# Kernel optimization log

Hardware: AMD Instinct MI355X
Metric: run time of the kernel (lower is better)

Reference implementation:

```python
import jax, jax.numpy as jnp
import numpy as np

HID, H, QR, KVR, DN, DR, DV = 2048, 20, 768, 512, 192, 64, 256
HEAD_DIM = DN + DR  # 256
EPS = 1e-5
THETA = 1000000.0
SCALE = 1.0 / np.sqrt(HEAD_DIM)


def rmsnorm(x, w):
    rms = jnp.sqrt(jnp.mean(x * x, axis=-1, keepdims=True) + EPS)
    return x / rms * w


def rope_apply(x, positions):
    # x: [B,S,H,DR], positions: [B,S] int
    inv_freq = 1.0 / (THETA ** (jnp.arange(0, DR, 2, dtype=jnp.float32) / DR))  # [DR/2]
    freqs = positions.astype(jnp.float32)[..., None] * inv_freq  # [B,S,DR/2]
    cos = jnp.cos(freqs)[:, :, None, :]  # [B,S,1,DR/2]
    sin = jnp.sin(freqs)[:, :, None, :]
    x1, x2 = x[..., ::2], x[..., 1::2]
    return jnp.concatenate([x1 * cos - x2 * sin, x1 * sin + x2 * cos], axis=-1)


def setup_inputs() -> dict:
    key = jax.random.key(0)
    ks = jax.random.split(key, 7)
    B, S = 1, 2048
    return {
        "x": jax.random.normal(ks[0], (B, S, HID), dtype=jnp.float32),
        "positions": jnp.tile(jnp.arange(S, dtype=jnp.int32)[None, :], (B, 1)),
        "q_a_w": jax.random.normal(ks[1], (QR, HID), dtype=jnp.float32) * 0.02,
        "q_b_w": jax.random.normal(ks[2], (H * HEAD_DIM, QR), dtype=jnp.float32) * 0.02,
        "kv_a_w": jax.random.normal(ks[3], (KVR + DR, HID), dtype=jnp.float32) * 0.02,
        "kv_b_w": jax.random.normal(ks[4], (H * (DN + DV), KVR), dtype=jnp.float32) * 0.02,
        "o_w": jax.random.normal(ks[5], (HID, H * DV), dtype=jnp.float32) * 0.02,
        "q_a_ln_w": jnp.ones((QR,), dtype=jnp.float32),
        "kv_a_ln_w": jnp.ones((KVR,), dtype=jnp.float32),
    }


def reference(x, positions, q_a_w, q_b_w, kv_a_w, kv_b_w, o_w, q_a_ln_w, kv_a_ln_w):
    B, S, _ = x.shape
    # Q: LoRA down -> RMSNorm -> up
    q = rmsnorm(x @ q_a_w.T, q_a_ln_w) @ q_b_w.T  # [B,S,H*HEAD_DIM]
    q = q.reshape(B, S, H, HEAD_DIM)
    # KV: compressed projection, split lora / rope-pe parts
    kv_c = x @ kv_a_w.T  # [B,S,KVR+DR]
    kv_lora, k_rope_pe = kv_c[..., :KVR], kv_c[..., KVR:]
    kv_exp = rmsnorm(kv_lora, kv_a_ln_w) @ kv_b_w.T  # [B,S,H*(DN+DV)]
    kv_exp = kv_exp.reshape(B, S, H, DN + DV)
    k_nope, v = kv_exp[..., :DN], kv_exp[..., DN:]
    k_rope = jnp.broadcast_to(k_rope_pe[:, :, None, :], (B, S, H, DR))
    q_nope, q_rope = q[..., :DN], q[..., DN:]
    q_rope = rope_apply(q_rope, positions)
    k_rope = rope_apply(k_rope, positions)
    qf = jnp.concatenate([q_nope, q_rope], axis=-1)  # [B,S,H,HEAD_DIM]
    kf = jnp.concatenate([k_nope, k_rope], axis=-1)
    # attention: manual matmul-softmax-matmul
    attn = jnp.einsum("bqhd,bkhd->bhqk", qf, kf) * SCALE
    attn = jax.nn.softmax(attn, axis=-1)
    out = jnp.einsum("bhqk,bkhd->bqhd", attn, v).reshape(B, S, H * DV)
    return out @ o_w.T
```

## Files before the change

### kernel.cpp

```cpp
#include <hip/hip_runtime.h>
#include <hip/hip_bf16.h>

#define HID 2048
#define NH 20
#define QR 768
#define KVR 512
#define DN 192
#define DR 64
#define DV 256
#define HD 256
#define S_LEN 2048
#define HKV 448
#define KV_N (NH * HKV)
#define Q_N (NH * HD)
#define O_N (NH * DV)
#define KVA_N (KVR + DR)
#define KVAP 640
#define QKVA (QR + KVAP)

typedef short bf16x8 __attribute__((ext_vector_type(8)));
typedef short bf16x4 __attribute__((ext_vector_type(4)));
typedef float f32x4 __attribute__((ext_vector_type(4)));

__device__ inline short f2bs(float f) {
  __hip_bfloat16 h = __float2bfloat16(f);
  return *reinterpret_cast<short*>(&h);
}
__device__ inline float bs2f(short s) {
  __hip_bfloat16 h = *reinterpret_cast<__hip_bfloat16*>(&s);
  return __bfloat162float(h);
}

__device__ inline void gload16(const void* g, void* l) {
  __builtin_amdgcn_global_load_lds((const __attribute__((address_space(1))) void*)g,
                                   (__attribute__((address_space(3))) void*)l, 16, 0, 0);
}

#define WAIT_VM0() asm volatile("s_waitcnt vmcnt(0)" ::: "memory")

__global__ void f2b_kernel(const float* __restrict__ in, short* __restrict__ out, size_t n8) {
  size_t i = (size_t)blockIdx.x * blockDim.x + threadIdx.x;
  size_t stride = (size_t)gridDim.x * blockDim.x;
  for (; i < n8; i += stride) {
    f32x4 a = *(const f32x4*)(in + i * 8);
    f32x4 b = *(const f32x4*)(in + i * 8 + 4);
    bf16x8 r;
    r[0] = f2bs(a[0]); r[1] = f2bs(a[1]); r[2] = f2bs(a[2]); r[3] = f2bs(a[3]);
    r[4] = f2bs(b[0]); r[5] = f2bs(b[1]); r[6] = f2bs(b[2]); r[7] = f2bs(b[3]);
    *(bf16x8*)(out + i * 8) = r;
  }
}

template <int OUT_BF16>
__global__ __launch_bounds__(256) void gemm128(const short* __restrict__ A,
                                               const short* __restrict__ B,
                                               void* __restrict__ Cp,
                                               int M, int N, int K) {
  __shared__ alignas(16) short As[128 * 64];
  __shared__ alignas(16) short Bs[128 * 64];
  int tid = threadIdx.x;
  int w = tid >> 6, l = tid & 63;
  int lr = l & 15, lg = l >> 4;
  int wr = w >> 1, wc = w & 1;
  int row0 = blockIdx.y * 128, col0 = blockIdx.x * 128;
  f32x4 acc[4][4] = {};
  for (int k0 = 0; k0 < K; k0 += 64) {
    if (k0) __syncthreads();
#pragma unroll
    for (int p = 0; p < 4; ++p) {
      int c = p * 256 + tid;
      int row = c >> 3;
      int sb = ((c & 7) * 16) ^ ((row & 7) << 4);
      gload16((const char*)A + ((size_t)(row0 + row) * K + k0) * 2 + sb, (char*)As + c * 16);
      gload16((const char*)B + ((size_t)(col0 + row) * K + k0) * 2 + sb, (char*)Bs + c * 16);
    }
    __syncthreads();
    bf16x8 af[4][2], bf[4][2];
#pragma unroll
    for (int m = 0; m < 4; ++m)
#pragma unroll
      for (int kk = 0; kk < 2; ++kk) {
        int ra = wr * 64 + m * 16 + lr;
        int rb = wc * 64 + m * 16 + lr;
        int cb = kk * 64 + lg * 16;
        af[m][kk] = *(const bf16x8*)((const char*)As + ra * 128 + (cb ^ ((ra & 7) << 4)));
        bf[m][kk] = *(const bf16x8*)((const char*)Bs + rb * 128 + (cb ^ ((rb & 7) << 4)));
      }
#pragma unroll
    for (int m = 0; m < 4; ++m)
#pragma unroll
      for (int n = 0; n < 4; ++n) {
        acc[m][n] = __builtin_amdgcn_mfma_f32_16x16x32_bf16(af[m][0], bf[n][0], acc[m][n], 0, 0, 0);
        acc[m][n] = __builtin_amdgcn_mfma_f32_16x16x32_bf16(af[m][1], bf[n][1], acc[m][n], 0, 0, 0);
      }
  }
#pragma unroll
  for (int m = 0; m < 4; ++m)
#pragma unroll
    for (int n = 0; n < 4; ++n)
#pragma unroll
      for (int r = 0; r < 4; ++r) {
        int row = row0 + wr * 64 + m * 16 + lg * 4 + r;
        int col = col0 + wc * 64 + n * 16 + lr;
        if (OUT_BF16)
          ((short*)Cp)[(size_t)row * N + col] = f2bs(acc[m][n][r]);
        else
          ((float*)Cp)[(size_t)row * N + col] = acc[m][n][r];
      }
}

__global__ __launch_bounds__(256) void gemm64(const short* __restrict__ A,
                                              const short* __restrict__ B,
                                              float* __restrict__ C,
                                              int M, int N, int K) {
  __shared__ alignas(16) short As[64 * 64];
  __shared__ alignas(16) short Bs[128 * 64];
  int tid = threadIdx.x;
  int w = tid >> 6, l = tid & 63;
  int lr = l & 15, lg = l >> 4;
  int wr = w >> 1, wc = w & 1;
  int row0 = blockIdx.y * 64, col0 = blockIdx.x * 128;
  f32x4 acc[2][4] = {};
  for (int k0 = 0; k0 < K; k0 += 64) {
    if (k0) __syncthreads();
#pragma unroll
    for (int p = 0; p < 2; ++p) {
      int c = p * 256 + tid;
      int row = c >> 3;
      int sb = ((c & 7) * 16) ^ ((row & 7) << 4);
      gload16((const char*)A + ((size_t)(row0 + row) * K + k0) * 2 + sb, (char*)As + c * 16);
    }
#pragma unroll
    for (int p = 0; p < 4; ++p) {
      int c = p * 256 + tid;
      int row = c >> 3;
      int sb = ((c & 7) * 16) ^ ((row & 7) << 4);
      gload16((const char*)B + ((size_t)(col0 + row) * K + k0) * 2 + sb, (char*)Bs + c * 16);
    }
    __syncthreads();
    bf16x8 af[2][2], bf[4][2];
#pragma unroll
    for (int m = 0; m < 2; ++m)
#pragma unroll
      for (int kk = 0; kk < 2; ++kk) {
        int ra = wr * 32 + m * 16 + lr;
        int cb = kk * 64 + lg * 16;
        af[m][kk] = *(const bf16x8*)((const char*)As + ra * 128 + (cb ^ ((ra & 7) << 4)));
      }
#pragma unroll
    for (int n = 0; n < 4; ++n)
#pragma unroll
      for (int kk = 0; kk < 2; ++kk) {
        int rb = wc * 64 + n * 16 + lr;
        int cb = kk * 64 + lg * 16;
        bf[n][kk] = *(const bf16x8*)((const char*)Bs + rb * 128 + (cb ^ ((rb & 7) << 4)));
      }
#pragma unroll
    for (int m = 0; m < 2; ++m)
#pragma unroll
      for (int n = 0; n < 4; ++n) {
        acc[m][n] = __builtin_amdgcn_mfma_f32_16x16x32_bf16(af[m][0], bf[n][0], acc[m][n], 0, 0, 0);
        acc[m][n] = __builtin_amdgcn_mfma_f32_16x16x32_bf16(af[m][1], bf[n][1], acc[m][n], 0, 0, 0);
      }
  }
#pragma unroll
  for (int m = 0; m < 2; ++m)
#pragma unroll
    for (int n = 0; n < 4; ++n)
#pragma unroll
      for (int r = 0; r < 4; ++r) {
        int row = row0 + wr * 32 + m * 16 + lg * 4 + r;
        int col = col0 + wc * 64 + n * 16 + lr;
        C[(size_t)row * N + col] = acc[m][n][r];
      }
}

__global__ __launch_bounds__(256) void rmsnorm_kernel(const float* __restrict__ in,
                                                      const float* __restrict__ w,
                                                      short* __restrict__ out,
                                                      int N, int in_stride, int out_stride) {
  int row = blockIdx.x;
  const float* x = in + (size_t)row * in_stride;
  float ss = 0.f;
  for (int i = threadIdx.x * 4; i < N; i += 1024) {
    f32x4 v = *(const f32x4*)(x + i);
    ss += v[0] * v[0] + v[1] * v[1] + v[2] * v[2] + v[3] * v[3];
  }
#pragma unroll
  for (int off = 32; off >= 1; off >>= 1) ss += __shfl_down(ss, off);
  __shared__ float red[4];
  if ((threadIdx.x & 63) == 0) red[threadIdx.x >> 6] = ss;
  __syncthreads();
  float tot = red[0] + red[1] + red[2] + red[3];
  float sc = rsqrtf(tot / (float)N + 1e-5f);
  short* o = out + (size_t)row * out_stride;
  for (int i = threadIdx.x * 4; i < N; i += 1024) {
    f32x4 v = *(const f32x4*)(x + i);
    f32x4 g = *(const f32x4*)(w + i);
    bf16x4 r;
    r[0] = f2bs(v[0] * sc * g[0]); r[1] = f2bs(v[1] * sc * g[1]);
    r[2] = f2bs(v[2] * sc * g[2]); r[3] = f2bs(v[3] * sc * g[3]);
    *(bf16x4*)(o + i) = r;
  }
}

__global__ void rope_table_kernel(const int* __restrict__ pos, float* __restrict__ ct,
                                  float* __restrict__ st) {
  int s = blockIdx.x * blockDim.x + threadIdx.x;
  if (s >= S_LEN) return;
  double p = (double)pos[s];
  for (int d = 0; d < 32; ++d) {
    double invf = exp(-((double)(2 * d) / 64.0) * log(1.0e6));
    double a = p * invf;
    ct[s * 32 + d] = (float)cos(a);
    st[s * 32 + d] = (float)sin(a);
  }
}

__global__ void rope_q_kernel(short* __restrict__ q, const float* __restrict__ ct,
                              const float* __restrict__ st) {
  int idx = blockIdx.x * blockDim.x + threadIdx.x;
  if (idx >= S_LEN * NH) return;
  int s = idx / NH, h = idx % NH;
  short* p = q + (size_t)s * Q_N + h * HD + DN;
  bf16x8 v[8];
#pragma unroll
  for (int j = 0; j < 8; ++j) v[j] = *(const bf16x8*)(p + j * 8);
  float x[64];
#pragma unroll
  for (int j = 0; j < 8; ++j)
#pragma unroll
    for (int k = 0; k < 8; ++k) x[j * 8 + k] = bs2f(v[j][k]);
  const float* c = ct + s * 32;
  const float* sn = st + s * 32;
  bf16x8 o[8];
#pragma unroll
  for (int d = 0; d < 32; ++d) {
    float cd = c[d], sd = sn[d];
    float x1 = x[2 * d], x2 = x[2 * d + 1];
    o[d >> 3][d & 7] = f2bs(x1 * cd - x2 * sd);
    o[4 + (d >> 3)][d & 7] = f2bs(x1 * sd + x2 * cd);
  }
#pragma unroll
  for (int j = 0; j < 8; ++j) *(bf16x8*)(p + j * 8) = o[j];
}

__global__ void rope_k_kernel(const float* __restrict__ base, const float* __restrict__ ct,
                              const float* __restrict__ st, short* __restrict__ kr) {
  int s = blockIdx.x * blockDim.x + threadIdx.x;
  if (s >= S_LEN) return;
  const float* xp = base + (size_t)s * QKVA;
  float x[64];
#pragma unroll
  for (int j = 0; j < 16; ++j) {
    f32x4 v = *(const f32x4*)(xp + j * 4);
    x[j * 4] = v[0]; x[j * 4 + 1] = v[1]; x[j * 4 + 2] = v[2]; x[j * 4 + 3] = v[3];
  }
  const float* c = ct + s * 32;
  const float* sn = st + s * 32;
  bf16x8 o[8];
#pragma unroll
  for (int d = 0; d < 32; ++d) {
    float cd = c[d], sd = sn[d];
    float x1 = x[2 * d], x2 = x[2 * d + 1];
    o[d >> 3][d & 7] = f2bs(x1 * cd - x2 * sd);
    o[4 + (d >> 3)][d & 7] = f2bs(x1 * sd + x2 * cd);
  }
  short* kp = kr + s * 64;
#pragma unroll
  for (int j = 0; j < 8; ++j) *(bf16x8*)(kp + j * 8) = o[j];
}

__global__ void kc_build(const short* __restrict__ kvx, const short* __restrict__ kr,
                         short* __restrict__ kc) {
  int idx = blockIdx.x * 256 + threadIdx.x;
  int h = idx >> 16;
  int r = idx & 65535;
  int s = r >> 5, c = r & 31;
  const short* src = (c < 24) ? kvx + (size_t)s * KV_N + h * HKV + c * 8
                              : kr + (size_t)s * 64 + (c - 24) * 8;
  *(bf16x8*)(kc + ((size_t)h * S_LEN + s) * HD + c * 8) = *(const bf16x8*)src;
}

__global__ __launch_bounds__(256) void vtrans(const short* __restrict__ kvx,
                                              short* __restrict__ vtg) {
  __shared__ short tile[64][65];
  int s0 = blockIdx.x * 64, d0 = blockIdx.y * 64, h = blockIdx.z;
  int tid = threadIdx.x;
#pragma unroll
  for (int p = 0; p < 2; ++p) {
    int s = p * 32 + (tid >> 3), dc = (tid & 7) * 8;
    bf16x8 v = *(const bf16x8*)(kvx + (size_t)(s0 + s) * KV_N + h * HKV + DN + d0 + dc);
#pragma unroll
    for (int j = 0; j < 8; ++j) tile[s][dc + j] = v[j];
  }
  __syncthreads();
#pragma unroll
  for (int p = 0; p < 2; ++p) {
    int d = p * 32 + (tid >> 3), sc = (tid & 7) * 8;
    bf16x4 a, b;
#pragma unroll
    for (int j = 0; j < 4; ++j) a[j] = tile[sc + j][d];
#pragma unroll
    for (int j = 0; j < 4; ++j) b[j] = tile[sc + 4 + j][d];
    int q1 = sc & 31, q2 = q1 + 4;
    int p1 = (q1 < 16) ? (q1 >> 2) * 8 : ((q1 - 16) >> 2) * 8 + 4;
    int p2 = (q2 < 16) ? (q2 >> 2) * 8 : ((q2 - 16) >> 2) * 8 + 4;
    int s = ((d & 15) >> 1) & 3;
    p1 = ((((p1 >> 3) ^ s)) << 3) | (p1 & 7);
    p2 = ((((p2 >> 3) ^ s)) << 3) | (p2 & 7);
    size_t rowbase = ((size_t)h * DV + d0 + d) * S_LEN + s0 + (sc & ~31);
    *(bf16x4*)(vtg + rowbase + p1) = a;
    *(bf16x4*)(vtg + rowbase + p2) = b;
  }
}

__global__ __launch_bounds__(256, 2) void attn10(const short* __restrict__ q,
                                                 const short* __restrict__ kc,
                                                 const short* __restrict__ vtg,
                                                 short* __restrict__ out) {
  __shared__ alignas(16) short ks[2][32 * 256];
  __shared__ alignas(16) short vt[2][256 * 32];
  int bid = blockIdx.x;
  int swz = (bid & 7) * 40 + (bid >> 3);
  int h = swz >> 4, qblk = swz & 15;
  int tid = threadIdx.x;
  int w = tid >> 6, l = tid & 63;
  int lr = l & 15, lg = l >> 4;

  const char* kch = (const char*)(kc + (size_t)h * S_LEN * HD);
  const short* vth = vtg + (size_t)h * DV * S_LEN;

  int qrowA = qblk * 128 + w * 32 + lr;
  const short* qbA = q + (size_t)qrowA * Q_N + h * HD;
  const short* qbB = qbA + (size_t)16 * Q_N;
  bf16x8 qfA[8], qfB[8];
#pragma unroll
  for (int kk = 0; kk < 8; ++kk) {
    bf16x8 va = *(const bf16x8*)(qbA + kk * 32 + lg * 8);
    bf16x8 vb = *(const bf16x8*)(qbB + kk * 32 + lg * 8);
#pragma unroll
    for (int j = 0; j < 8; ++j) {
      va[j] = f2bs(bs2f(va[j]) * 0.0625f);
      vb[j] = f2bs(bs2f(vb[j]) * 0.0625f);
    }
    qfA[kk] = va;
    qfB[kk] = vb;
  }

  f32x4 accA[16] = {}, accB[16] = {};
  float mA = -3e38f, mB = -3e38f;
  float lsA = 0.f, lsB = 0.f;

  auto stage_k = [&](int buf, int key0) {
#pragma unroll
    for (int p = 0; p < 4; ++p) {
      int c = p * 256 + tid;
      int row = c >> 5;
      int sb = ((c & 31) * 16) ^ ((row & 7) << 4);
      gload16(kch + (size_t)(key0 + row) * 512 + sb, (char*)ks[buf] + c * 16);
    }
  };
  auto stage_v = [&](int buf, int key0) {
#pragma unroll
    for (int p = 0; p < 4; ++p) {
      int c = p * 256 + tid;
      int d = c >> 2, slot = c & 3;
      gload16(vth + (size_t)d * S_LEN + key0 + slot * 8, (char*)vt[buf] + c * 16);
    }
  };

  stage_k(0, 0);
  stage_v(0, 0);
  WAIT_VM0();
  __builtin_amdgcn_s_barrier();

  int sxor = (lr >> 1) & 3;

  for (int kb = 0; kb < S_LEN / 32; ++kb) {
    int cur = kb & 1;
    int key0 = kb * 32;
    if (kb + 1 < S_LEN / 32) {
      stage_k(cur ^ 1, key0 + 32);
      stage_v(cur ^ 1, key0 + 32);
    }

    f32x4 s0A = {}, s1A = {}, s0B = {}, s1B = {};
    __builtin_amdgcn_s_setprio(1);
#pragma unroll
    for (int kk = 0; kk < 8; ++kk) {
      int cb = kk * 64 + lg * 16;
      int sw = (lr & 7) << 4;
      bf16x8 k0 = *(const bf16x8*)((const char*)ks[cur] + lr * 512 + (cb ^ sw));
      bf16x8 k1 = *(const bf16x8*)((const char*)ks[cur] + (16 + lr) * 512 + (cb ^ sw));
      s0A = __builtin_amdgcn_mfma_f32_16x16x32_bf16(k0, qfA[kk], s0A, 0, 0, 0);
      s1A = __builtin_amdgcn_mfma_f32_16x16x32_bf16(k1, qfA[kk], s1A, 0, 0, 0);
      s0B = __builtin_amdgcn_mfma_f32_16x16x32_bf16(k0, qfB[kk], s0B, 0, 0, 0);
      s1B = __builtin_amdgcn_mfma_f32_16x16x32_bf16(k1, qfB[kk], s1B, 0, 0, 0);
    }
    __builtin_amdgcn_s_setprio(0);

    bf16x8 paA, paB;
    {
      float mx = fmaxf(fmaxf(fmaxf(s0A[0], s0A[1]), fmaxf(s0A[2], s0A[3])),
                       fmaxf(fmaxf(s1A[0], s1A[1]), fmaxf(s1A[2], s1A[3])));
      mx = fmaxf(mx, __shfl_xor(mx, 16));
      mx = fmaxf(mx, __shfl_xor(mx, 32));
      bool grow = mx > mA + 8.f;
      if (__any((int)grow)) {
        float mn = fmaxf(mA, mx);
        float co = __expf(mA - mn);
        mA = mn;
        lsA *= co;
        float c0 = __shfl(co, (l & 48) | (lg * 4 + 0));
        float c1 = __shfl(co, (l & 48) | (lg * 4 + 1));
        float c2 = __shfl(co, (l & 48) | (lg * 4 + 2));
        float c3 = __shfl(co, (l & 48) | (lg * 4 + 3));
#pragma unroll
        for (int t = 0; t < 16; ++t) {
          accA[t][0] *= c0; accA[t][1] *= c1; accA[t][2] *= c2; accA[t][3] *= c3;
        }
      }
      float e0 = __expf(s0A[0] - mA), e1 = __expf(s0A[1] - mA);
      float e2 = __expf(s0A[2] - mA), e3 = __expf(s0A[3] - mA);
      float e4 = __expf(s1A[0] - mA), e5 = __expf(s1A[1] - mA);
      float e6 = __expf(s1A[2] - mA), e7 = __expf(s1A[3] - mA);
      float ts = ((e0 + e1) + (e2 + e3)) + ((e4 + e5) + (e6 + e7));
      ts += __shfl_xor(ts, 16);
      ts += __shfl_xor(ts, 32);
      lsA += ts;
      paA[0] = f2bs(e0); paA[1] = f2bs(e1); paA[2] = f2bs(e2); paA[3] = f2bs(e3);
      paA[4] = f2bs(e4); paA[5] = f2bs(e5); paA[6] = f2bs(e6); paA[7] = f2bs(e7);
    }
    {
      float mx = fmaxf(fmaxf(fmaxf(s0B[0], s0B[1]), fmaxf(s0B[2], s0B[3])),
                       fmaxf(fmaxf(s1B[0], s1B[1]), fmaxf(s1B[2], s1B[3])));
      mx = fmaxf(mx, __shfl_xor(mx, 16));
      mx = fmaxf(mx, __shfl_xor(mx, 32));
      bool grow = mx > mB + 8.f;
      if (__any((int)grow)) {
        float mn = fmaxf(mB, mx);
        float co = __expf(mB - mn);
        mB = mn;
        lsB *= co;
        float c0 = __shfl(co, (l & 48) | (lg * 4 + 0));
        float c1 = __shfl(co, (l & 48) | (lg * 4 + 1));
        float c2 = __shfl(co, (l & 48) | (lg * 4 + 2));
        float c3 = __shfl(co, (l & 48) | (lg * 4 + 3));
#pragma unroll
        for (int t = 0; t < 16; ++t) {
          accB[t][0] *= c0; accB[t][1] *= c1; accB[t][2] *= c2; accB[t][3] *= c3;
        }
      }
      float e0 = __expf(s0B[0] - mB), e1 = __expf(s0B[1] - mB);
      float e2 = __expf(s0B[2] - mB), e3 = __expf(s0B[3] - mB);
      float e4 = __expf(s1B[0] - mB), e5 = __expf(s1B[1] - mB);
      float e6 = __expf(s1B[2] - mB), e7 = __expf(s1B[3] - mB);
      float ts = ((e0 + e1) + (e2 + e3)) + ((e4 + e5) + (e6 + e7));
      ts += __shfl_xor(ts, 16);
      ts += __shfl_xor(ts, 32);
      lsB += ts;
      paB[0] = f2bs(e0); paB[1] = f2bs(e1); paB[2] = f2bs(e2); paB[3] = f2bs(e3);
      paB[4] = f2bs(e4); paB[5] = f2bs(e5); paB[6] = f2bs(e6); paB[7] = f2bs(e7);
    }

    __builtin_amdgcn_s_setprio(1);
#pragma unroll
    for (int t = 0; t < 16; ++t) {
      int d = t * 16 + lr;
      bf16x8 vf = *(const bf16x8*)((const char*)vt[cur] + d * 64 + ((lg ^ sxor) << 4));
      accA[t] = __builtin_amdgcn_mfma_f32_16x16x32_bf16(paA, vf, accA[t], 0, 0, 0);
      accB[t] = __builtin_amdgcn_mfma_f32_16x16x32_bf16(paB, vf, accB[t], 0, 0, 0);
    }
    __builtin_amdgcn_s_setprio(0);

    WAIT_VM0();
    __builtin_amdgcn_s_barrier();
  }

  {
    float inv = 1.f / lsA;
    float i0 = __shfl(inv, (l & 48) | (lg * 4 + 0));
    float i1 = __shfl(inv, (l & 48) | (lg * 4 + 1));
    float i2 = __shfl(inv, (l & 48) | (lg * 4 + 2));
    float i3 = __shfl(inv, (l & 48) | (lg * 4 + 3));
#pragma unroll
    for (int t = 0; t < 16; ++t) {
      int row = qblk * 128 + w * 32 + lg * 4;
      int col = h * DV + t * 16 + lr;
      out[(size_t)(row + 0) * O_N + col] = f2bs(accA[t][0] * i0);
      out[(size_t)(row + 1) * O_N + col] = f2bs(accA[t][1] * i1);
      out[(size_t)(row + 2) * O_N + col] = f2bs(accA[t][2] * i2);
      out[(size_t)(row + 3) * O_N + col] = f2bs(accA[t][3] * i3);
    }
  }
  {
    float inv = 1.f / lsB;
    float i0 = __shfl(inv, (l & 48) | (lg * 4 + 0));
    float i1 = __shfl(inv, (l & 48) | (lg * 4 + 1));
    float i2 = __shfl(inv, (l & 48) | (lg * 4 + 2));
    float i3 = __shfl(inv, (l & 48) | (lg * 4 + 3));
#pragma unroll
    for (int t = 0; t < 16; ++t) {
      int row = qblk * 128 + w * 32 + 16 + lg * 4;
      int col = h * DV + t * 16 + lr;
      out[(size_t)(row + 0) * O_N + col] = f2bs(accB[t][0] * i0);
      out[(size_t)(row + 1) * O_N + col] = f2bs(accB[t][1] * i1);
      out[(size_t)(row + 2) * O_N + col] = f2bs(accB[t][2] * i2);
      out[(size_t)(row + 3) * O_N + col] = f2bs(accB[t][3] * i3);
    }
  }
}

extern "C" void kernel_launch(void* const* d_in, const int* in_sizes, int n_in,
                              void* d_out, int out_size, void* d_ws, size_t ws_size,
                              hipStream_t stream) {
  const float* x       = (const float*)d_in[0];
  const int*   pos     = (const int*)d_in[1];
  const float* q_a_w   = (const float*)d_in[2];
  const float* q_b_w   = (const float*)d_in[3];
  const float* kv_a_w  = (const float*)d_in[4];
  const float* kv_b_w  = (const float*)d_in[5];
  const float* o_w     = (const float*)d_in[6];
  const float* q_a_ln  = (const float*)d_in[7];
  const float* kv_a_ln = (const float*)d_in[8];
  float* out = (float*)d_out;

  char* p = (char*)d_ws;
  auto alloc = [&](size_t bytes) {
    char* r = p;
    p += (bytes + 255) & ~(size_t)255;
    return r;
  };
  short* xb    = (short*)alloc((size_t)S_LEN * HID * 2);
  short* wcat  = (short*)alloc((size_t)QKVA * HID * 2);
  short* qbw   = (short*)alloc((size_t)Q_N * QR * 2);
  short* kvbw  = (short*)alloc((size_t)KV_N * KVR * 2);
  short* ow    = (short*)alloc((size_t)HID * O_N * 2);
  float* qkv   = (float*)alloc((size_t)S_LEN * QKVA * 4);
  short* q_ln  = (short*)alloc((size_t)S_LEN * QR * 2);
  short* qbuf  = (short*)alloc((size_t)S_LEN * Q_N * 2);
  short* kv_ln = (short*)alloc((size_t)S_LEN * KVR * 2);
  short* kvx   = (short*)alloc((size_t)S_LEN * KV_N * 2);
  short* kr    = (short*)alloc((size_t)S_LEN * 64 * 2);
  float* ct    = (float*)alloc((size_t)S_LEN * 32 * 4);
  float* st    = (float*)alloc((size_t)S_LEN * 32 * 4);
  short* ao    = (short*)alloc((size_t)S_LEN * O_N * 2);
  short* kcb   = (short*)alloc((size_t)NH * S_LEN * HD * 2);
  short* vtg   = (short*)alloc((size_t)NH * DV * S_LEN * 2);
  (void)ws_size; (void)n_in; (void)in_sizes; (void)out_size;

  auto cvt = [&](const float* in, short* o, size_t n) {
    size_t n8 = n / 8;
    size_t blocks = (n8 + 255) / 256;
    if (blocks > 2048) blocks = 2048;
    f2b_kernel<<<dim3((unsigned)blocks), dim3(256), 0, stream>>>(in, o, n8);
  };
  cvt(x, xb, (size_t)S_LEN * HID);
  cvt(q_a_w, wcat, (size_t)QR * HID);
  cvt(kv_a_w, wcat + (size_t)QR * HID, (size_t)KVA_N * HID);
  hipMemsetAsync(wcat + (size_t)(QR + KVA_N) * HID, 0, (size_t)(KVAP - KVA_N) * HID * 2, stream);
  cvt(q_b_w, qbw, (size_t)Q_N * QR);
  cvt(kv_b_w, kvbw, (size_t)KV_N * KVR);
  cvt(o_w, ow, (size_t)HID * O_N);

  dim3 blk(256);
  gemm64<<<dim3(QKVA / 128, S_LEN / 64), blk, 0, stream>>>(xb, wcat, qkv, S_LEN, QKVA, HID);
  rmsnorm_kernel<<<dim3(S_LEN), blk, 0, stream>>>(qkv, q_a_ln, q_ln, QR, QKVA, QR);
  rmsnorm_kernel<<<dim3(S_LEN), blk, 0, stream>>>(qkv + QR, kv_a_ln, kv_ln, KVR, QKVA, KVR);
  gemm128<1><<<dim3(Q_N / 128, S_LEN / 128), blk, 0, stream>>>(q_ln, qbw, qbuf, S_LEN, Q_N, QR);
  gemm128<1><<<dim3(KV_N / 128, S_LEN / 128), blk, 0, stream>>>(kv_ln, kvbw, kvx, S_LEN, KV_N, KVR);
  rope_table_kernel<<<dim3(S_LEN / 256), blk, 0, stream>>>(pos, ct, st);
  rope_q_kernel<<<dim3((S_LEN * NH + 255) / 256), blk, 0, stream>>>(qbuf, ct, st);
  rope_k_kernel<<<dim3(S_LEN / 256), blk, 0, stream>>>(qkv + QR + KVR, ct, st, kr);
  kc_build<<<dim3(NH * S_LEN * 32 / 256), blk, 0, stream>>>(kvx, kr, kcb);
  vtrans<<<dim3(S_LEN / 64, DV / 64, NH), blk, 0, stream>>>(kvx, vtg);
  attn10<<<dim3(NH * S_LEN / 128), blk, 0, stream>>>(qbuf, kcb, vtg, ao);
  gemm64<<<dim3(HID / 128, S_LEN / 64), blk, 0, stream>>>(ao, ow, out, S_LEN, HID, O_N);
}
```

Baseline: 386.7 us.

## Split attention keys in two with persistent atomic work queue and combine pass

The attention kernel becomes a persistent kernel of 512 blocks that pull (head, query block, key half) items from an atomic counter. Each item processes half the key range and writes unnormalized fp32 partial accumulators plus running max and sum. A new combine kernel merges the two halves into the bf16 output. This targets tail imbalance from 320 blocks on 256 CUs, at the cost of extra fp32 partial traffic (about 84MB written and read), a second kernel launch, and Q fragments loaded twice. The fp32 partial buffer reuses workspace from earlier buffers that are dead by then.

```diff
diff --git a/kernel.cpp b/kernel.cpp
--- a/kernel.cpp
+++ b/kernel.cpp
@@ -17,6 +17,7 @@
 #define KVA_N (KVR + DR)
 #define KVAP 640
 #define QKVA (QR + KVAP)
+#define N_ITEMS (2 * NH * 16)
 
 typedef short bf16x8 __attribute__((ext_vector_type(8)));
 typedef short bf16x4 __attribute__((ext_vector_type(4)));
@@ -315,201 +316,222 @@
   }
 }
 
-__global__ __launch_bounds__(256, 2) void attn10(const short* __restrict__ q,
+__global__ __launch_bounds__(256, 2) void attn11(const short* __restrict__ q,
                                                  const short* __restrict__ kc,
                                                  const short* __restrict__ vtg,
-                                                 short* __restrict__ out) {
+                                                 float* __restrict__ pacc,
+                                                 float* __restrict__ pm,
+                                                 float* __restrict__ pl,
+                                                 int* __restrict__ counter) {
   __shared__ alignas(16) short ks[2][32 * 256];
   __shared__ alignas(16) short vt[2][256 * 32];
-  int bid = blockIdx.x;
-  int swz = (bid & 7) * 40 + (bid >> 3);
-  int h = swz >> 4, qblk = swz & 15;
+  __shared__ int item_s;
   int tid = threadIdx.x;
   int w = tid >> 6, l = tid & 63;
   int lr = l & 15, lg = l >> 4;
-
-  const char* kch = (const char*)(kc + (size_t)h * S_LEN * HD);
-  const short* vth = vtg + (size_t)h * DV * S_LEN;
-
-  int qrowA = qblk * 128 + w * 32 + lr;
-  const short* qbA = q + (size_t)qrowA * Q_N + h * HD;
-  const short* qbB = qbA + (size_t)16 * Q_N;
-  bf16x8 qfA[8], qfB[8];
-#pragma unroll
-  for (int kk = 0; kk < 8; ++kk) {
-    bf16x8 va = *(const bf16x8*)(qbA + kk * 32 + lg * 8);
-    bf16x8 vb = *(const bf16x8*)(qbB + kk * 32 + lg * 8);
-#pragma unroll
-    for (int j = 0; j < 8; ++j) {
-      va[j] = f2bs(bs2f(va[j]) * 0.0625f);
-      vb[j] = f2bs(bs2f(vb[j]) * 0.0625f);
+  int sxor = (lr >> 1) & 3;
+
+  for (;;) {
+    if (tid == 0) item_s = atomicAdd(counter, 1);
+    __syncthreads();
+    int item = item_s;
+    if (item >= N_ITEMS) return;
+    int khalf = item & 1;
+    int hq = item >> 1;
+    int h = hq >> 4, qblk = hq & 15;
+
+    const char* kch = (const char*)(kc + (size_t)h * S_LEN * HD);
+    const short* vth = vtg + (size_t)h * DV * S_LEN;
+
+    int qrowA = qblk * 128 + w * 32 + lr;
+    const short* qbA = q + (size_t)qrowA * Q_N + h * HD;
+    const short* qbB = qbA + (size_t)16 * Q_N;
+    bf16x8 qfA[8], qfB[8];
+#pragma unroll
+    for (int kk = 0; kk < 8; ++kk) {
+      bf16x8 va = *(const bf16x8*)(qbA + kk * 32 + lg * 8);
+      bf16x8 vb = *(const bf16x8*)(qbB + kk * 32 + lg * 8);
+#pragma unroll
+      for (int j = 0; j < 8; ++j) {
+        va[j] = f2bs(bs2f(va[j]) * 0.0625f);
+        vb[j] = f2bs(bs2f(vb[j]) * 0.0625f);
+      }
+      qfA[kk] = va;
+      qfB[kk] = vb;
     }
-    qfA[kk] = va;
-    qfB[kk] = vb;
-  }
-
-  f32x4 accA[16] = {}, accB[16] = {};
-  float mA = -3e38f, mB = -3e38f;
-  float lsA = 0.f, lsB = 0.f;
-
-  auto stage_k = [&](int buf, int key0) {
-#pragma unroll
-    for (int p = 0; p < 4; ++p) {
-      int c = p * 256 + tid;
-      int row = c >> 5;
-      int sb = ((c & 31) * 16) ^ ((row & 7) << 4);
-      gload16(kch + (size_t)(key0 + row) * 512 + sb, (char*)ks[buf] + c * 16);
-    }
-  };
-  auto stage_v = [&](int buf, int key0) {
-#pragma unroll
-    for (int p = 0; p < 4; ++p) {
-      int c = p * 256 + tid;
-      int d = c >> 2, slot = c & 3;
-      gload16(vth + (size_t)d * S_LEN + key0 + slot * 8, (char*)vt[buf] + c * 16);
-    }
-  };
-
-  stage_k(0, 0);
-  stage_v(0, 0);
-  WAIT_VM0();
-  __builtin_amdgcn_s_barrier();
-
-  int sxor = (lr >> 1) & 3;
-
-  for (int kb = 0; kb < S_LEN / 32; ++kb) {
-    int cur = kb & 1;
-    int key0 = kb * 32;
-    if (kb + 1 < S_LEN / 32) {
-      stage_k(cur ^ 1, key0 + 32);
-      stage_v(cur ^ 1, key0 + 32);
-    }
-
-    f32x4 s0A = {}, s1A = {}, s0B = {}, s1B = {};
-    __builtin_amdgcn_s_setprio(1);
-#pragma unroll
-    for (int kk = 0; kk < 8; ++kk) {
-      int cb = kk * 64 + lg * 16;
-      int sw = (lr & 7) << 4;
-      bf16x8 k0 = *(const bf16x8*)((const char*)ks[cur] + lr * 512 + (cb ^ sw));
-      bf16x8 k1 = *(const bf16x8*)((const char*)ks[cur] + (16 + lr) * 512 + (cb ^ sw));
-      s0A = __builtin_amdgcn_mfma_f32_16x16x32_bf16(k0, qfA[kk], s0A, 0, 0, 0);
-      s1A = __builtin_amdgcn_mfma_f32_16x16x32_bf16(k1, qfA[kk], s1A, 0, 0, 0);
-      s0B = __builtin_amdgcn_mfma_f32_16x16x32_bf16(k0, qfB[kk], s0B, 0, 0, 0);
-      s1B = __builtin_amdgcn_mfma_f32_16x16x32_bf16(k1, qfB[kk], s1B, 0, 0, 0);
-    }
-    __builtin_amdgcn_s_setprio(0);
-
-    bf16x8 paA, paB;
-    {
-      float mx = fmaxf(fmaxf(fmaxf(s0A[0], s0A[1]), fmaxf(s0A[2], s0A[3])),
-                       fmaxf(fmaxf(s1A[0], s1A[1]), fmaxf(s1A[2], s1A[3])));
-      mx = fmaxf(mx, __shfl_xor(mx, 16));
-      mx = fmaxf(mx, __shfl_xor(mx, 32));
-      bool grow = mx > mA + 8.f;
-      if (__any((int)grow)) {
-        float mn = fmaxf(mA, mx);
-        float co = __expf(mA - mn);
-        mA = mn;
-        lsA *= co;
-        float c0 = __shfl(co, (l & 48) | (lg * 4 + 0));
-        float c1 = __shfl(co, (l & 48) | (lg * 4 + 1));
-        float c2 = __shfl(co, (l & 48) | (lg * 4 + 2));
-        float c3 = __shfl(co, (l & 48) | (lg * 4 + 3));
-#pragma unroll
-        for (int t = 0; t < 16; ++t) {
-          accA[t][0] *= c0; accA[t][1] *= c1; accA[t][2] *= c2; accA[t][3] *= c3;
-        }
-      }
-      float e0 = __expf(s0A[0] - mA), e1 = __expf(s0A[1] - mA);
-      float e2 = __expf(s0A[2] - mA), e3 = __expf(s0A[3] - mA);
-      float e4 = __expf(s1A[0] - mA), e5 = __expf(s1A[1] - mA);
-      float e6 = __expf(s1A[2] - mA), e7 = __expf(s1A[3] - mA);
-      float ts = ((e0 + e1) + (e2 + e3)) + ((e4 + e5) + (e6 + e7));
-      ts += __shfl_xor(ts, 16);
-      ts += __shfl_xor(ts, 32);
-      lsA += ts;
-      paA[0] = f2bs(e0); paA[1] = f2bs(e1); paA[2] = f2bs(e2); paA[3] = f2bs(e3);
-      paA[4] = f2bs(e4); paA[5] = f2bs(e5); paA[6] = f2bs(e6); paA[7] = f2bs(e7);
-    }
-    {
-      float mx = fmaxf(fmaxf(fmaxf(s0B[0], s0B[1]), fmaxf(s0B[2], s0B[3])),
-                       fmaxf(fmaxf(s1B[0], s1B[1]), fmaxf(s1B[2], s1B[3])));
-      mx = fmaxf(mx, __shfl_xor(mx, 16));
-      mx = fmaxf(mx, __shfl_xor(mx, 32));
-      bool grow = mx > mB + 8.f;
-      if (__any((int)grow)) {
-        float mn = fmaxf(mB, mx);
-        float co = __expf(mB - mn);
-        mB = mn;
-        lsB *= co;
-        float c0 = __shfl(co, (l & 48) | (lg * 4 + 0));
-        float c1 = __shfl(co, (l & 48) | (lg * 4 + 1));
-        float c2 = __shfl(co, (l & 48) | (lg * 4 + 2));
-        float c3 = __shfl(co, (l & 48) | (lg * 4 + 3));
-#pragma unroll
-        for (int t = 0; t < 16; ++t) {
-          accB[t][0] *= c0; accB[t][1] *= c1; accB[t][2] *= c2; accB[t][3] *= c3;
-        }
-      }
-      float e0 = __expf(s0B[0] - mB), e1 = __expf(s0B[1] - mB);
-      float e2 = __expf(s0B[2] - mB), e3 = __expf(s0B[3] - mB);
-      float e4 = __expf(s1B[0] - mB), e5 = __expf(s1B[1] - mB);
-      float e6 = __expf(s1B[2] - mB), e7 = __expf(s1B[3] - mB);
-      float ts = ((e0 + e1) + (e2 + e3)) + ((e4 + e5) + (e6 + e7));
-      ts += __shfl_xor(ts, 16);
-      ts += __shfl_xor(ts, 32);
-      lsB += ts;
-      paB[0] = f2bs(e0); paB[1] = f2bs(e1); paB[2] = f2bs(e2); paB[3] = f2bs(e3);
-      paB[4] = f2bs(e4); paB[5] = f2bs(e5); paB[6] = f2bs(e6); paB[7] = f2bs(e7);
-    }
-
-    __builtin_amdgcn_s_setprio(1);
-#pragma unroll
-    for (int t = 0; t < 16; ++t) {
-      int d = t * 16 + lr;
-      bf16x8 vf = *(const bf16x8*)((const char*)vt[cur] + d * 64 + ((lg ^ sxor) << 4));
-      accA[t] = __builtin_amdgcn_mfma_f32_16x16x32_bf16(paA, vf, accA[t], 0, 0, 0);
-      accB[t] = __builtin_amdgcn_mfma_f32_16x16x32_bf16(paB, vf, accB[t], 0, 0, 0);
-    }
-    __builtin_amdgcn_s_setprio(0);
-
+
+    f32x4 accA[16] = {}, accB[16] = {};
+    float mA = -3e38f, mB = -3e38f;
+    float lsA = 0.f, lsB = 0.f;
+
+    auto stage_k = [&](int buf, int key0) {
+#pragma unroll
+      for (int p = 0; p < 4; ++p) {
+        int c = p * 256 + tid;
+        int row = c >> 5;
+        int sb = ((c & 31) * 16) ^ ((row & 7) << 4);
+        gload16(kch + (size_t)(key0 + row) * 512 + sb, (char*)ks[buf] + c * 16);
+      }
+    };
+    auto stage_v = [&](int buf, int key0) {
+#pragma unroll
+      for (int p = 0; p < 4; ++p) {
+        int c = p * 256 + tid;
+        int d = c >> 2, slot = c & 3;
+        gload16(vth + (size_t)d * S_LEN + key0 + slot * 8, (char*)vt[buf] + c * 16);
+      }
+    };
+
+    int kb0 = khalf * 32, kbE = kb0 + 32;
+    stage_k(0, kb0 * 32);
+    stage_v(0, kb0 * 32);
     WAIT_VM0();
     __builtin_amdgcn_s_barrier();
-  }
-
-  {
-    float inv = 1.f / lsA;
-    float i0 = __shfl(inv, (l & 48) | (lg * 4 + 0));
-    float i1 = __shfl(inv, (l & 48) | (lg * 4 + 1));
-    float i2 = __shfl(inv, (l & 48) | (lg * 4 + 2));
-    float i3 = __shfl(inv, (l & 48) | (lg * 4 + 3));
+
+    for (int kb = kb0; kb < kbE; ++kb) {
+      int cur = kb & 1;
+      int key0 = kb * 32;
+      if (kb + 1 < kbE) {
+        stage_k(cur ^ 1, key0 + 32);
+        stage_v(cur ^ 1, key0 + 32);
+      }
+
+      f32x4 s0A = {}, s1A = {}, s0B = {}, s1B = {};
+      __builtin_amdgcn_s_setprio(1);
+#pragma unroll
+      for (int kk = 0; kk < 8; ++kk) {
+        int cb = kk * 64 + lg * 16;
+        int sw = (lr & 7) << 4;
+        bf16x8 k0 = *(const bf16x8*)((const char*)ks[cur] + lr * 512 + (cb ^ sw));
+        bf16x8 k1 = *(const bf16x8*)((const char*)ks[cur] + (16 + lr) * 512 + (cb ^ sw));
+        s0A = __builtin_amdgcn_mfma_f32_16x16x32_bf16(k0, qfA[kk], s0A, 0, 0, 0);
+        s1A = __builtin_amdgcn_mfma_f32_16x16x32_bf16(k1, qfA[kk], s1A, 0, 0, 0);
+        s0B = __builtin_amdgcn_mfma_f32_16x16x32_bf16(k0, qfB[kk], s0B, 0, 0, 0);
+        s1B = __builtin_amdgcn_mfma_f32_16x16x32_bf16(k1, qfB[kk], s1B, 0, 0, 0);
+      }
+      __builtin_amdgcn_s_setprio(0);
+
+      bf16x8 paA, paB;
+      {
+        float mx = fmaxf(fmaxf(fmaxf(s0A[0], s0A[1]), fmaxf(s0A[2], s0A[3])),
+                         fmaxf(fmaxf(s1A[0], s1A[1]), fmaxf(s1A[2], s1A[3])));
+        mx = fmaxf(mx, __shfl_xor(mx, 16));
+        mx = fmaxf(mx, __shfl_xor(mx, 32));
+        bool grow = mx > mA + 8.f;
+        if (__any((int)grow)) {
+          float mn = fmaxf(mA, mx);
+          float co = __expf(mA - mn);
+          mA = mn;
+          lsA *= co;
+          float c0 = __shfl(co, (l & 48) | (lg * 4 + 0));
+          float c1 = __shfl(co, (l & 48) | (lg * 4 + 1));
+          float c2 = __shfl(co, (l & 48) | (lg * 4 + 2));
+          float c3 = __shfl(co, (l & 48) | (lg * 4 + 3));
+#pragma unroll
+          for (int t = 0; t < 16; ++t) {
+            accA[t][0] *= c0; accA[t][1] *= c1; accA[t][2] *= c2; accA[t][3] *= c3;
+          }
+        }
+        float e0 = __expf(s0A[0] - mA), e1 = __expf(s0A[1] - mA);
+        float e2 = __expf(s0A[2] - mA), e3 = __expf(s0A[3] - mA);
+        float e4 = __expf(s1A[0] - mA), e5 = __expf(s1A[1] - mA);
+        float e6 = __expf(s1A[2] - mA), e7 = __expf(s1A[3] - mA);
+        float ts = ((e0 + e1) + (e2 + e3)) + ((e4 + e5) + (e6 + e7));
+        ts += __shfl_xor(ts, 16);
+        ts += __shfl_xor(ts, 32);
+        lsA += ts;
+        paA[0] = f2bs(e0); paA[1] = f2bs(e1); paA[2] = f2bs(e2); paA[3] = f2bs(e3);
+        paA[4] = f2bs(e4); paA[5] = f2bs(e5); paA[6] = f2bs(e6); paA[7] = f2bs(e7);
+      }
+      {
+        float mx = fmaxf(fmaxf(fmaxf(s0B[0], s0B[1]), fmaxf(s0B[2], s0B[3])),
+                         fmaxf(fmaxf(s1B[0], s1B[1]), fmaxf(s1B[2], s1B[3])));
+        mx = fmaxf(mx, __shfl_xor(mx, 16));
+        mx = fmaxf(mx, __shfl_xor(mx, 32));
+        bool grow = mx > mB + 8.f;
+        if (__any((int)grow)) {
+          float mn = fmaxf(mB, mx);
+          float co = __expf(mB - mn);
+          mB = mn;
+          lsB *= co;
+          float c0 = __shfl(co, (l & 48) | (lg * 4 + 0));
+          float c1 = __shfl(co, (l & 48) | (lg * 4 + 1));
+          float c2 = __shfl(co, (l & 48) | (lg * 4 + 2));
+          float c3 = __shfl(co, (l & 48) | (lg * 4 + 3));
+#pragma unroll
+          for (int t = 0; t < 16; ++t) {
+            accB[t][0] *= c0; accB[t][1] *= c1; accB[t][2] *= c2; accB[t][3] *= c3;
+          }
+        }
+        float e0 = __expf(s0B[0] - mB), e1 = __expf(s0B[1] - mB);
+        float e2 = __expf(s0B[2] - mB), e3 = __expf(s0B[3] - mB);
+        float e4 = __expf(s1B[0] - mB), e5 = __expf(s1B[1] - mB);
+        float e6 = __expf(s1B[2] - mB), e7 = __expf(s1B[3] - mB);
+        float ts = ((e0 + e1) + (e2 + e3)) + ((e4 + e5) + (e6 + e7));
+        ts += __shfl_xor(ts, 16);
+        ts += __shfl_xor(ts, 32);
+        lsB += ts;
+        paB[0] = f2bs(e0); paB[1] = f2bs(e1); paB[2] = f2bs(e2); paB[3] = f2bs(e3);
+        paB[4] = f2bs(e4); paB[5] = f2bs(e5); paB[6] = f2bs(e6); paB[7] = f2bs(e7);
+      }
+
+      __builtin_amdgcn_s_setprio(1);
+#pragma unroll
+      for (int t = 0; t < 16; ++t) {
+        int d = t * 16 + lr;
+        bf16x8 vf = *(const bf16x8*)((const char*)vt[cur] + d * 64 + ((lg ^ sxor) << 4));
+        accA[t] = __builtin_amdgcn_mfma_f32_16x16x32_bf16(paA, vf, accA[t], 0, 0, 0);
+        accB[t] = __builtin_amdgcn_mfma_f32_16x16x32_bf16(paB, vf, accB[t], 0, 0, 0);
+      }
+      __builtin_amdgcn_s_setprio(0);
+
+      WAIT_VM0();
+      __builtin_amdgcn_s_barrier();
+    }
+
+    size_t probA = (size_t)(khalf * NH + h) * S_LEN + qblk * 128 + w * 32;
 #pragma unroll
     for (int t = 0; t < 16; ++t) {
-      int row = qblk * 128 + w * 32 + lg * 4;
-      int col = h * DV + t * 16 + lr;
-      out[(size_t)(row + 0) * O_N + col] = f2bs(accA[t][0] * i0);
-      out[(size_t)(row + 1) * O_N + col] = f2bs(accA[t][1] * i1);
-      out[(size_t)(row + 2) * O_N + col] = f2bs(accA[t][2] * i2);
-      out[(size_t)(row + 3) * O_N + col] = f2bs(accA[t][3] * i3);
+      float* pp = pacc + (probA + lg * 4) * 256 + t * 16 + lr;
+      pp[0] = accA[t][0]; pp[256] = accA[t][1]; pp[512] = accA[t][2]; pp[768] = accA[t][3];
+      float* pq = pacc + (probA + 16 + lg * 4) * 256 + t * 16 + lr;
+      pq[0] = accB[t][0]; pq[256] = accB[t][1]; pq[512] = accB[t][2]; pq[768] = accB[t][3];
     }
-  }
-  {
-    float inv = 1.f / lsB;
-    float i0 = __shfl(inv, (l & 48) | (lg * 4 + 0));
-    float i1 = __shfl(inv, (l & 48) | (lg * 4 + 1));
-    float i2 = __shfl(inv, (l & 48) | (lg * 4 + 2));
-    float i3 = __shfl(inv, (l & 48) | (lg * 4 + 3));
-#pragma unroll
-    for (int t = 0; t < 16; ++t) {
-      int row = qblk * 128 + w * 32 + 16 + lg * 4;
-      int col = h * DV + t * 16 + lr;
-      out[(size_t)(row + 0) * O_N + col] = f2bs(accB[t][0] * i0);
-      out[(size_t)(row + 1) * O_N + col] = f2bs(accB[t][1] * i1);
-      out[(size_t)(row + 2) * O_N + col] = f2bs(accB[t][2] * i2);
-      out[(size_t)(row + 3) * O_N + col] = f2bs(accB[t][3] * i3);
+    if (lg == 0) {
+      pm[probA + lr] = mA;
+      pl[probA + lr] = lsA;
+      pm[probA + 16 + lr] = mB;
+      pl[probA + 16 + lr] = lsB;
     }
   }
+}
+
+__global__ __launch_bounds__(256) void combine_kernel(const float* __restrict__ pacc,
+                                                      const float* __restrict__ pm,
+                                                      const float* __restrict__ pl,
+                                                      short* __restrict__ ao) {
+  int gt = blockIdx.x * 256 + threadIdx.x;
+  int dg = gt & 31;
+  int rh = gt >> 5;
+  int h = rh >> 11, row = rh & 2047;
+  size_t i1 = (size_t)h * S_LEN + row;
+  size_t i2 = (size_t)(NH + h) * S_LEN + row;
+  float m1 = pm[i1], m2 = pm[i2];
+  float l1 = pl[i1], l2 = pl[i2];
+  float M = fmaxf(m1, m2);
+  float e1 = __expf(m1 - M), e2 = __expf(m2 - M);
+  float inv = 1.f / (e1 * l1 + e2 * l2);
+  float w1 = e1 * inv, w2 = e2 * inv;
+  const float* a1 = pacc + i1 * 256 + dg * 8;
+  const float* a2 = pacc + i2 * 256 + dg * 8;
+  f32x4 x1a = *(const f32x4*)a1, x1b = *(const f32x4*)(a1 + 4);
+  f32x4 x2a = *(const f32x4*)a2, x2b = *(const f32x4*)(a2 + 4);
+  bf16x8 r;
+#pragma unroll
+  for (int j = 0; j < 4; ++j) r[j] = f2bs(x1a[j] * w1 + x2a[j] * w2);
+#pragma unroll
+  for (int j = 0; j < 4; ++j) r[4 + j] = f2bs(x1b[j] * w1 + x2b[j] * w2);
+  *(bf16x8*)(ao + (size_t)row * O_N + h * DV + dg * 8) = r;
 }
 
 extern "C" void kernel_launch(void* const* d_in, const int* in_sizes, int n_in,
@@ -526,28 +548,33 @@
   const float* kv_a_ln = (const float*)d_in[8];
   float* out = (float*)d_out;
 
-  char* p = (char*)d_ws;
-  auto alloc = [&](size_t bytes) {
-    char* r = p;
-    p += (bytes + 255) & ~(size_t)255;
-    return r;
-  };
-  short* xb    = (short*)alloc((size_t)S_LEN * HID * 2);
-  short* wcat  = (short*)alloc((size_t)QKVA * HID * 2);
-  short* qbw   = (short*)alloc((size_t)Q_N * QR * 2);
-  short* kvbw  = (short*)alloc((size_t)KV_N * KVR * 2);
-  short* ow    = (short*)alloc((size_t)HID * O_N * 2);
-  float* qkv   = (float*)alloc((size_t)S_LEN * QKVA * 4);
-  short* q_ln  = (short*)alloc((size_t)S_LEN * QR * 2);
-  short* qbuf  = (short*)alloc((size_t)S_LEN * Q_N * 2);
-  short* kv_ln = (short*)alloc((size_t)S_LEN * KVR * 2);
-  short* kvx   = (short*)alloc((size_t)S_LEN * KV_N * 2);
-  short* kr    = (short*)alloc((size_t)S_LEN * 64 * 2);
-  float* ct    = (float*)alloc((size_t)S_LEN * 32 * 4);
-  float* st    = (float*)alloc((size_t)S_LEN * 32 * 4);
-  short* ao    = (short*)alloc((size_t)S_LEN * O_N * 2);
-  short* kcb   = (short*)alloc((size_t)NH * S_LEN * HD * 2);
-  short* vtg   = (short*)alloc((size_t)NH * DV * S_LEN * 2);
+  char* base = (char*)d_ws;
+  auto align256 = [](size_t v) { return (v + 255) & ~(size_t)255; };
+  size_t offA = 0;
+  auto allocA = [&](size_t bytes) { char* r = base + offA; offA = align256(offA + bytes); return r; };
+  short* xb    = (short*)allocA((size_t)S_LEN * HID * 2);
+  short* wcat  = (short*)allocA((size_t)QKVA * HID * 2);
+  short* qbw   = (short*)allocA((size_t)Q_N * QR * 2);
+  short* kvbw  = (short*)allocA((size_t)KV_N * KVR * 2);
+  float* qkv   = (float*)allocA((size_t)S_LEN * QKVA * 4);
+  short* q_ln  = (short*)allocA((size_t)S_LEN * QR * 2);
+  short* kv_ln = (short*)allocA((size_t)S_LEN * KVR * 2);
+  short* kvx   = (short*)allocA((size_t)S_LEN * KV_N * 2);
+  short* kr    = (short*)allocA((size_t)S_LEN * 64 * 2);
+  float* ct    = (float*)allocA((size_t)S_LEN * 32 * 4);
+  float* st    = (float*)allocA((size_t)S_LEN * 32 * 4);
+  float* pacc  = (float*)base;
+  size_t paccB = (size_t)2 * NH * S_LEN * 256 * 4;
+  size_t offB = align256(offA > paccB ? offA : paccB);
+  auto allocB = [&](size_t bytes) { char* r = base + offB; offB = align256(offB + bytes); return r; };
+  short* ow    = (short*)allocB((size_t)HID * O_N * 2);
+  short* qbuf  = (short*)allocB((size_t)S_LEN * Q_N * 2);
+  short* kcb   = (short*)allocB((size_t)NH * S_LEN * HD * 2);
+  short* vtg   = (short*)allocB((size_t)NH * DV * S_LEN * 2);
+  short* ao    = (short*)allocB((size_t)S_LEN * O_N * 2);
+  float* pm    = (float*)allocB((size_t)2 * NH * S_LEN * 4);
+  float* pl    = (float*)allocB((size_t)2 * NH * S_LEN * 4);
+  int*   cnt   = (int*)allocB(256);
   (void)ws_size; (void)n_in; (void)in_sizes; (void)out_size;
 
   auto cvt = [&](const float* in, short* o, size_t n) {
@@ -575,6 +602,8 @@
   rope_k_kernel<<<dim3(S_LEN / 256), blk, 0, stream>>>(qkv + QR + KVR, ct, st, kr);
   kc_build<<<dim3(NH * S_LEN * 32 / 256), blk, 0, stream>>>(kvx, kr, kcb);
   vtrans<<<dim3(S_LEN / 64, DV / 64, NH), blk, 0, stream>>>(kvx, vtg);
-  attn10<<<dim3(NH * S_LEN / 128), blk, 0, stream>>>(qbuf, kcb, vtg, ao);
+  hipMemsetAsync(cnt, 0, 4, stream);
+  attn11<<<dim3(512), blk, 0, stream>>>(qbuf, kcb, vtg, pacc, pm, pl, cnt);
+  combine_kernel<<<dim3(S_LEN * NH * DV / (8 * 256)), blk, 0, stream>>>(pacc, pm, pl, ao);
   gemm64<<<dim3(HID / 128, S_LEN / 64), blk, 0, stream>>>(ao, ow, out, S_LEN, HID, O_N);
 }
```

Measured after the change: 444.1 us. 1.15x slower.
